# Kernel optimization log

Hardware: AMD Instinct MI355X
Metric: run time of the kernel (lower is better)

The kernel has to match this reference:

```python
import jax, jax.numpy as jnp
import numpy as np

N_NODES = 100_000
DEG = 16
N_EDGES = N_NODES * DEG
NODE_F = 128
EDGE_F = 16
HID = 64
B = 64
K = DEG


def setup_inputs() -> dict:
    key = jax.random.key(0)
    ks = jax.random.split(key, 12)
    # node i's outgoing edges are at ids i + k*N_NODES for k in [0, DEG)
    src = jnp.arange(N_EDGES, dtype=jnp.int32) % N_NODES
    dst = jax.random.randint(ks[0], (N_EDGES,), 0, N_NODES, dtype=jnp.int32)
    edge_index = jnp.stack([src, dst])
    current_nodes = jax.random.randint(ks[1], (B,), 0, N_NODES, dtype=jnp.int32)
    # reachable neighbors = destinations of the current node's real edges
    neighbor_nodes = dst[current_nodes[:, None] + jnp.arange(K, dtype=jnp.int32)[None, :] * N_NODES]
    x = jax.random.normal(ks[2], (N_NODES, NODE_F), jnp.float32)
    edge_attr = jax.random.normal(ks[3], (N_EDGES, EDGE_F), jnp.float32)
    return dict(
        x=x,
        edge_attr=edge_attr,
        conv1_W=jax.random.normal(ks[4], (NODE_F, HID), jnp.float32) * (NODE_F ** -0.5),
        conv1_b=jnp.zeros((HID,), jnp.float32),
        conv2_W=jax.random.normal(ks[5], (HID, HID), jnp.float32) * (HID ** -0.5),
        conv2_b=jnp.zeros((HID,), jnp.float32),
        mlp_W1=jax.random.normal(ks[6], (2 * HID + EDGE_F, 2 * HID), jnp.float32) * ((2 * HID + EDGE_F) ** -0.5),
        mlp_b1=jnp.zeros((2 * HID,), jnp.float32),
        mlp_W2=jax.random.normal(ks[7], (2 * HID, 1), jnp.float32) * ((2 * HID) ** -0.5),
        mlp_b2=jnp.zeros((1,), jnp.float32),
        edge_index=edge_index,
        current_nodes=current_nodes,
        neighbor_nodes=neighbor_nodes,
    )


def gcn_conv(x, edge_index, W, b):
    """PyG GCNConv: symmetric norm with self-loops, then linear + bias."""
    n = x.shape[0]
    loop = jnp.arange(n, dtype=edge_index.dtype)
    src = jnp.concatenate([edge_index[0], loop])  # messages flow src -> dst
    dst = jnp.concatenate([edge_index[1], loop])
    xw = x @ W                                    # [N, H]
    deg = jnp.zeros((n,), xw.dtype).at[dst].add(1.0)
    dinv = jnp.where(deg > 0, jax.lax.rsqrt(deg), 0.0)
    msg = (dinv[src] * dinv[dst])[:, None] * xw[src]      # [E+N, H]
    return jax.ops.segment_sum(msg, dst, num_segments=n) + b


def reference(x, edge_attr, conv1_W, conv1_b, conv2_W, conv2_b,
              mlp_W1, mlp_b1, mlp_W2, mlp_b2,
              edge_index, current_nodes, neighbor_nodes):
    n = x.shape[0]
    h = jax.nn.relu(gcn_conv(x, edge_index, conv1_W, conv1_b))
    h = jax.nn.relu(gcn_conv(h, edge_index, conv2_W, conv2_b))

    # First edge id matching each (current, neighbor) pair, replacing the
    # original O(E)-per-neighbor boolean-mask loop with a sorted-key lookup.
    keys = edge_index[0].astype(jnp.int64) * n + edge_index[1].astype(jnp.int64)
    order = jnp.argsort(keys, stable=True)        # stable -> leftmost == first edge id
    skeys = keys[order]
    query = current_nodes[:, None].astype(jnp.int64) * n + neighbor_nodes.astype(jnp.int64)
    pos = jnp.clip(jnp.searchsorted(skeys, query), 0, skeys.shape[0] - 1)
    valid = skeys[pos] == query                   # [B, K]
    eid = order[pos]
    ea = edge_attr[eid]                           # [B, K, F]

    b_, k_ = neighbor_nodes.shape
    h_cur = jnp.broadcast_to(h[current_nodes][:, None, :], (b_, k_, h.shape[1]))
    h_nbr = h[neighbor_nodes]
    m = jnp.concatenate([h_cur, h_nbr, ea], axis=-1)  # [B, K, 2H+F]
    q = (jax.nn.relu(m @ mlp_W1 + mlp_b1) @ mlp_W2 + mlp_b2)[..., 0]
    q = jnp.where(valid, q, 0.0)
    return q, valid
```

## Files before the change

kernel.cpp:

```cpp
#include <hip/hip_runtime.h>

#define N_NODES 100000
#define DEG 16
#define N_EDGES (N_NODES * DEG)
#define NODE_F 128
#define EDGE_F 16
#define HID 64
#define NQ 1024
#define NCHUNK (N_EDGES / 256)
#define XTILES ((N_NODES + 63) / 64)
#define BCAP 56
#define NODE_BLOCKS (N_NODES / 4)

__global__ void k_query(const int* __restrict__ dst, const int* __restrict__ cur,
                        const int* __restrict__ nbr, int* __restrict__ n1,
                        int* __restrict__ n2, int* __restrict__ eid_sel,
                        float* __restrict__ out_valid) {
  int i = blockIdx.x * blockDim.x + threadIdx.x;
  if (i >= NQ) return;
  int b = i >> 4;
  int c = cur[b];
  int nb = nbr[i];
  int sel = -1;
  #pragma unroll
  for (int j = 0; j < DEG; ++j) {
    int e = c + j * N_NODES;
    if (sel < 0 && dst[e] == nb) sel = e;
  }
  eid_sel[i] = sel;
  out_valid[i] = (sel >= 0) ? 1.0f : 0.0f;
  n2[c] = 1; n2[nb] = 1;
  n1[c] = 1; n1[nb] = 1;
}

__global__ void k_scan(const int* __restrict__ dst, const int* __restrict__ n2,
                       int* __restrict__ n1, int* __restrict__ deg) {
  int e = blockIdx.x * blockDim.x + threadIdx.x;
  if (e >= N_EDGES) return;
  int d = dst[e];
  atomicAdd(&deg[d], 1);
  if (n2[d]) n1[e % N_NODES] = 1;
}

__global__ void k_dinv(const int* __restrict__ deg, float* __restrict__ dinv) {
  int v = blockIdx.x * blockDim.x + threadIdx.x;
  if (v < N_NODES) dinv[v] = rsqrtf((float)(deg[v] + 1));
}

__global__ void k_bucket(const int* __restrict__ dst, const int* __restrict__ n1,
                         int* __restrict__ wcur, int* __restrict__ bucket) {
  int e = blockIdx.x * blockDim.x + threadIdx.x;
  if (e >= N_EDGES) return;
  int d = dst[e];
  if (!n1[d]) return;
  int pos = atomicAdd(&wcur[d], 1);
  if (pos < BCAP) bucket[(size_t)d * BCAP + pos] = e % N_NODES;
}

__global__ __launch_bounds__(256) void k_xw1(const float* __restrict__ x,
                                             const float* __restrict__ Wg,
                                             float* __restrict__ xw) {
  __shared__ float xs[64 * 129];
  const int t = threadIdx.x;
  const int lane = t & 63;
  const int w = __builtin_amdgcn_readfirstlane(t >> 6);
  const long base = (long)blockIdx.x * 64;

  const float4* __restrict__ xv = (const float4*)x;
  #pragma unroll
  for (int p = 0; p < 8; ++p) {
    int f4 = p * 256 + t;
    int r = f4 >> 5;
    int c4 = f4 & 31;
    long gr = base + r;
    float4 v = make_float4(0.f, 0.f, 0.f, 0.f);
    if (gr < N_NODES) v = xv[gr * 32 + c4];
    float* d = &xs[r * 129 + (c4 << 2)];
    d[0] = v.x; d[1] = v.y; d[2] = v.z; d[3] = v.w;
  }
  __syncthreads();

  float acc[16];
  #pragma unroll
  for (int j = 0; j < 16; ++j) acc[j] = 0.f;
  const float* __restrict__ wp = Wg + w * 16;
  #pragma unroll 4
  for (int k = 0; k < NODE_F; ++k) {
    float xk = xs[lane * 129 + k];
    float wv[16];
    #pragma unroll
    for (int j = 0; j < 16; ++j) wv[j] = wp[k * HID + j];
    #pragma unroll
    for (int j = 0; j < 16; ++j) acc[j] = fmaf(xk, wv[j], acc[j]);
  }
  long gr = base + lane;
  if (gr < N_NODES) {
    float* __restrict__ op = xw + gr * HID + w * 16;
    #pragma unroll
    for (int j = 0; j < 16; ++j) op[j] = acc[j];
  }
}

__global__ void k_xw2(const float* __restrict__ h1, const float* __restrict__ Wg,
                      const int* __restrict__ n1, float* __restrict__ xw2) {
  const int lane = threadIdx.x & 63;
  const int row = (blockIdx.x * blockDim.x + threadIdx.x) >> 6;
  if (row >= N_NODES) return;
  if (!n1[row]) return;
  const float* __restrict__ hr = h1 + (size_t)row * HID;
  float acc = 0.f;
  #pragma unroll
  for (int k = 0; k < HID; ++k) acc = fmaf(hr[k], Wg[k * HID + lane], acc);
  xw2[(size_t)row * HID + lane] = acc;
}

__global__ __launch_bounds__(256) void k_gather(
    const int* __restrict__ bucket, const int* __restrict__ wcur,
    const int* __restrict__ flag, const float* __restrict__ dinv,
    const float* __restrict__ xw, const float* __restrict__ bias,
    float* __restrict__ hout) {
  const int t = threadIdx.x;
  const int lane = t & 63;
  const int v = blockIdx.x * 4 + (t >> 6);
  if (v >= N_NODES) return;
  if (!flag[v]) return;
  int n = wcur[v];
  if (n > BCAP) n = BCAP;
  int   s_l = (lane < n) ? bucket[(size_t)v * BCAP + lane] : 0;
  float w_l = (lane < n) ? dinv[s_l] : 0.f;
  float acc = 0.f;
  int j = 0;
  for (; j + 3 < n; j += 4) {
    int s0 = __shfl(s_l, j);
    int s1 = __shfl(s_l, j + 1);
    int s2 = __shfl(s_l, j + 2);
    int s3 = __shfl(s_l, j + 3);
    float a0 = xw[(size_t)s0 * HID + lane];
    float a1 = xw[(size_t)s1 * HID + lane];
    float a2 = xw[(size_t)s2 * HID + lane];
    float a3 = xw[(size_t)s3 * HID + lane];
    acc = fmaf(__shfl(w_l, j), a0, acc);
    acc = fmaf(__shfl(w_l, j + 1), a1, acc);
    acc = fmaf(__shfl(w_l, j + 2), a2, acc);
    acc = fmaf(__shfl(w_l, j + 3), a3, acc);
  }
  for (; j < n; ++j)
    acc = fmaf(__shfl(w_l, j), xw[(size_t)__shfl(s_l, j) * HID + lane], acc);
  float dv = dinv[v];
  acc = fmaf(dv, xw[(size_t)v * HID + lane], acc);
  hout[(size_t)v * HID + lane] = fmaxf(fmaf(dv, acc, bias[lane]), 0.f);
}

__global__ void k_mlp(const float* __restrict__ h2, const float* __restrict__ ea,
                      const float* __restrict__ W1, const float* __restrict__ b1,
                      const float* __restrict__ W2, const float* __restrict__ b2,
                      const int* __restrict__ cur, const int* __restrict__ nbr,
                      const int* __restrict__ eid_sel, float* __restrict__ out) {
  __shared__ float m[2 * HID + EDGE_F];
  __shared__ float red[128];
  const int q = blockIdx.x;
  const int t = threadIdx.x;
  const int eid = eid_sel[q];
  if (eid < 0) {
    if (t == 0) out[q] = 0.0f;
    return;
  }
  const int b = q >> 4;
  const int c = cur[b];
  const int nb = nbr[q];
  if (t < HID)    m[t] = h2[(size_t)c * HID + t];
  else            m[t] = h2[(size_t)nb * HID + (t - HID)];
  if (t < EDGE_F) m[2 * HID + t] = ea[(size_t)eid * EDGE_F + t];
  __syncthreads();
  float h = b1[t];
  #pragma unroll
  for (int j = 0; j < 2 * HID + EDGE_F; ++j) h = fmaf(m[j], W1[j * 128 + t], h);
  h = fmaxf(h, 0.f) * W2[t];
  red[t] = h;
  __syncthreads();
  if (t < 64) {
    float v = red[t] + red[t + 64];
    #pragma unroll
    for (int o = 32; o > 0; o >>= 1) v += __shfl_down(v, o);
    if (t == 0) out[q] = v + b2[0];
  }
}

extern "C" void kernel_launch(void* const* d_in, const int* in_sizes, int n_in,
                              void* d_out, int out_size, void* d_ws, size_t ws_size,
                              hipStream_t stream) {
  const float* x    = (const float*)d_in[0];
  const float* ea   = (const float*)d_in[1];
  const float* c1W  = (const float*)d_in[2];
  const float* c1b  = (const float*)d_in[3];
  const float* c2W  = (const float*)d_in[4];
  const float* c2b  = (const float*)d_in[5];
  const float* mW1  = (const float*)d_in[6];
  const float* mb1  = (const float*)d_in[7];
  const float* mW2  = (const float*)d_in[8];
  const float* mb2  = (const float*)d_in[9];
  const int*   eidx = (const int*)d_in[10];
  const int*   cur  = (const int*)d_in[11];
  const int*   nbr  = (const int*)d_in[12];
  const int* edst = eidx + N_EDGES;
  float* out = (float*)d_out;

  char* p = (char*)d_ws;
  auto alloc = [&](size_t bytes) -> void* {
    void* r = (void*)p;
    p += (bytes + 255) & ~(size_t)255;
    return r;
  };
  int*   deg     = (int*)alloc((size_t)N_NODES * 4);
  float* dinv    = (float*)alloc((size_t)N_NODES * 4);
  int*   n1      = (int*)alloc((size_t)N_NODES * 4);
  int*   n2      = (int*)alloc((size_t)N_NODES * 4);
  int*   wcur    = (int*)alloc((size_t)N_NODES * 4);
  int*   eid_sel = (int*)alloc((size_t)NQ * 4);
  int*   bucket  = (int*)alloc((size_t)N_NODES * BCAP * 4);
  float* xw1     = (float*)alloc((size_t)N_NODES * HID * 4);
  float* h1      = (float*)alloc((size_t)N_NODES * HID * 4);
  float* xw2     = (float*)alloc((size_t)N_NODES * HID * 4);
  float* h2      = xw1;

  hipMemsetAsync(deg, 0, (size_t)N_NODES * 4, stream);
  hipMemsetAsync(n1, 0, (size_t)N_NODES * 4, stream);
  hipMemsetAsync(n2, 0, (size_t)N_NODES * 4, stream);
  hipMemsetAsync(wcur, 0, (size_t)N_NODES * 4, stream);

  k_query<<<(NQ + 255) / 256, 256, 0, stream>>>(edst, cur, nbr, n1, n2, eid_sel,
                                                out + NQ);
  k_scan<<<NCHUNK, 256, 0, stream>>>(edst, n2, n1, deg);
  k_dinv<<<(N_NODES + 255) / 256, 256, 0, stream>>>(deg, dinv);
  k_xw1<<<XTILES, 256, 0, stream>>>(x, c1W, xw1);
  k_bucket<<<NCHUNK, 256, 0, stream>>>(edst, n1, wcur, bucket);
  k_gather<<<NODE_BLOCKS, 256, 0, stream>>>(bucket, wcur, n1, dinv, xw1, c1b, h1);
  k_xw2<<<(N_NODES * HID + 255) / 256, 256, 0, stream>>>(h1, c2W, n1, xw2);
  k_gather<<<NODE_BLOCKS, 256, 0, stream>>>(bucket, wcur, n2, dinv, xw2, c2b, h2);
  k_mlp<<<NQ, 128, 0, stream>>>(h2, ea, mW1, mb1, mW2, mb2, cur, nbr, eid_sel, out);
}
```

Baseline: 380.4 us.

## Fuse graph preprocessing kernels, privatize degree histogram, replace flag memsets with sentinel

Four memsets and two separate launches are dropped. Node flags now use a magic sentinel value instead of being zeroed, and bucket counters are reset only for the nodes that get flagged. The degree histogram is split across 8 private copies, zeroed inside the query kernel, and computed in the same launch as the first-layer x@W GEMM so the two independent jobs overlap. The dinv computation shares a launch with bucketing. The aim is to cut launch and memset overhead and atomic contention, at the cost of relying on stale workspace never holding the sentinel and of leaving flags from earlier calls in place.

```diff
diff --git a/kernel.cpp b/kernel.cpp
--- a/kernel.cpp
+++ b/kernel.cpp
@@ -9,14 +9,25 @@
 #define NQ 1024
 #define NCHUNK (N_EDGES / 256)
 #define XTILES ((N_NODES + 63) / 64)
+#define NHIST 4096
 #define BCAP 56
-#define NODE_BLOCKS (N_NODES / 4)
-
-__global__ void k_query(const int* __restrict__ dst, const int* __restrict__ cur,
-                        const int* __restrict__ nbr, int* __restrict__ n1,
-                        int* __restrict__ n2, int* __restrict__ eid_sel,
-                        float* __restrict__ out_valid) {
-  int i = blockIdx.x * blockDim.x + threadIdx.x;
+#define NDINV ((N_NODES + 255) / 256)
+#define MAGIC 0x13579BDF
+
+__global__ void k_query_zero(const int* __restrict__ dst, const int* __restrict__ cur,
+                             const int* __restrict__ nbr, int* __restrict__ n1,
+                             int* __restrict__ n2, int* __restrict__ wcur,
+                             int* __restrict__ eid_sel, float* __restrict__ out_valid,
+                             int* __restrict__ degp) {
+  if (blockIdx.x >= 4) {
+    int4* d4 = (int4*)degp;
+    const int n4 = 8 * N_NODES / 4;
+    int i = (blockIdx.x - 4) * 256 + threadIdx.x;
+    const int stride = (gridDim.x - 4) * 256;
+    for (; i < n4; i += stride) d4[i] = make_int4(0, 0, 0, 0);
+    return;
+  }
+  int i = blockIdx.x * 256 + threadIdx.x;
   if (i >= NQ) return;
   int b = i >> 4;
   int c = cur[b];
@@ -29,42 +40,36 @@
   }
   eid_sel[i] = sel;
   out_valid[i] = (sel >= 0) ? 1.0f : 0.0f;
-  n2[c] = 1; n2[nb] = 1;
-  n1[c] = 1; n1[nb] = 1;
-}
-
-__global__ void k_scan(const int* __restrict__ dst, const int* __restrict__ n2,
-                       int* __restrict__ n1, int* __restrict__ deg) {
-  int e = blockIdx.x * blockDim.x + threadIdx.x;
-  if (e >= N_EDGES) return;
-  int d = dst[e];
-  atomicAdd(&deg[d], 1);
-  if (n2[d]) n1[e % N_NODES] = 1;
-}
-
-__global__ void k_dinv(const int* __restrict__ deg, float* __restrict__ dinv) {
-  int v = blockIdx.x * blockDim.x + threadIdx.x;
-  if (v < N_NODES) dinv[v] = rsqrtf((float)(deg[v] + 1));
-}
-
-__global__ void k_bucket(const int* __restrict__ dst, const int* __restrict__ n1,
-                         int* __restrict__ wcur, int* __restrict__ bucket) {
-  int e = blockIdx.x * blockDim.x + threadIdx.x;
-  if (e >= N_EDGES) return;
-  int d = dst[e];
-  if (!n1[d]) return;
-  int pos = atomicAdd(&wcur[d], 1);
-  if (pos < BCAP) bucket[(size_t)d * BCAP + pos] = e % N_NODES;
-}
-
-__global__ __launch_bounds__(256) void k_xw1(const float* __restrict__ x,
-                                             const float* __restrict__ Wg,
-                                             float* __restrict__ xw) {
+  n2[c] = MAGIC; n2[nb] = MAGIC;
+  n1[c] = MAGIC; n1[nb] = MAGIC;
+  wcur[c] = 0;   wcur[nb] = 0;
+}
+
+__global__ __launch_bounds__(256) void k_fusedA(
+    const float* __restrict__ x, const float* __restrict__ Wg,
+    float* __restrict__ xw, const int* __restrict__ dst,
+    const int* __restrict__ n2, int* __restrict__ n1, int* __restrict__ wcur,
+    int* __restrict__ degp) {
   __shared__ float xs[64 * 129];
   const int t = threadIdx.x;
+
+  if (blockIdx.x < NHIST) {
+    int* __restrict__ dp = degp + (size_t)(blockIdx.x & 7) * N_NODES;
+    for (int e = blockIdx.x * 256 + t; e < N_EDGES; e += NHIST * 256) {
+      int d = dst[e];
+      atomicAdd(&dp[d], 1);
+      if (n2[d] == MAGIC) {
+        int s = e % N_NODES;
+        n1[s] = MAGIC;
+        wcur[s] = 0;
+      }
+    }
+    return;
+  }
+
   const int lane = t & 63;
   const int w = __builtin_amdgcn_readfirstlane(t >> 6);
-  const long base = (long)blockIdx.x * 64;
+  const long base = (long)(blockIdx.x - NHIST) * 64;
 
   const float4* __restrict__ xv = (const float4*)x;
   #pragma unroll
@@ -101,12 +106,33 @@
   }
 }
 
+__global__ void k_bucket_dinv(const int* __restrict__ dst, const int* __restrict__ n1,
+                              int* __restrict__ wcur, int* __restrict__ bucket,
+                              const int* __restrict__ degp, float* __restrict__ dinv) {
+  if (blockIdx.x < NDINV) {
+    int v = blockIdx.x * 256 + threadIdx.x;
+    if (v < N_NODES) {
+      int s = 1;
+      #pragma unroll
+      for (int p = 0; p < 8; ++p) s += degp[(size_t)p * N_NODES + v];
+      dinv[v] = rsqrtf((float)s);
+    }
+    return;
+  }
+  int e = (blockIdx.x - NDINV) * 256 + threadIdx.x;
+  int d = dst[e];
+  if (n1[d] != MAGIC) return;
+  int pos = atomicAdd(&wcur[d], 1);
+  if (pos >= 0 && pos < BCAP)
+    bucket[(size_t)d * BCAP + pos] = e % N_NODES;
+}
+
 __global__ void k_xw2(const float* __restrict__ h1, const float* __restrict__ Wg,
                       const int* __restrict__ n1, float* __restrict__ xw2) {
   const int lane = threadIdx.x & 63;
   const int row = (blockIdx.x * blockDim.x + threadIdx.x) >> 6;
   if (row >= N_NODES) return;
-  if (!n1[row]) return;
+  if (n1[row] != MAGIC) return;
   const float* __restrict__ hr = h1 + (size_t)row * HID;
   float acc = 0.f;
   #pragma unroll
@@ -123,9 +149,10 @@
   const int lane = t & 63;
   const int v = blockIdx.x * 4 + (t >> 6);
   if (v >= N_NODES) return;
-  if (!flag[v]) return;
+  if (flag[v] != MAGIC) return;
   int n = wcur[v];
   if (n > BCAP) n = BCAP;
+  if (n < 0) n = 0;
   int   s_l = (lane < n) ? bucket[(size_t)v * BCAP + lane] : 0;
   float w_l = (lane < n) ? dinv[s_l] : 0.f;
   float acc = 0.f;
@@ -211,7 +238,7 @@
     p += (bytes + 255) & ~(size_t)255;
     return r;
   };
-  int*   deg     = (int*)alloc((size_t)N_NODES * 4);
+  int*   degp    = (int*)alloc((size_t)8 * N_NODES * 4);
   float* dinv    = (float*)alloc((size_t)N_NODES * 4);
   int*   n1      = (int*)alloc((size_t)N_NODES * 4);
   int*   n2      = (int*)alloc((size_t)N_NODES * 4);
@@ -223,19 +250,16 @@
   float* xw2     = (float*)alloc((size_t)N_NODES * HID * 4);
   float* h2      = xw1;
 
-  hipMemsetAsync(deg, 0, (size_t)N_NODES * 4, stream);
-  hipMemsetAsync(n1, 0, (size_t)N_NODES * 4, stream);
-  hipMemsetAsync(n2, 0, (size_t)N_NODES * 4, stream);
-  hipMemsetAsync(wcur, 0, (size_t)N_NODES * 4, stream);
-
-  k_query<<<(NQ + 255) / 256, 256, 0, stream>>>(edst, cur, nbr, n1, n2, eid_sel,
-                                                out + NQ);
-  k_scan<<<NCHUNK, 256, 0, stream>>>(edst, n2, n1, deg);
-  k_dinv<<<(N_NODES + 255) / 256, 256, 0, stream>>>(deg, dinv);
-  k_xw1<<<XTILES, 256, 0, stream>>>(x, c1W, xw1);
-  k_bucket<<<NCHUNK, 256, 0, stream>>>(edst, n1, wcur, bucket);
-  k_gather<<<NODE_BLOCKS, 256, 0, stream>>>(bucket, wcur, n1, dinv, xw1, c1b, h1);
+  k_query_zero<<<260, 256, 0, stream>>>(edst, cur, nbr, n1, n2, wcur, eid_sel,
+                                        out + NQ, degp);
+  k_fusedA<<<NHIST + XTILES, 256, 0, stream>>>(x, c1W, xw1, edst, n2, n1, wcur,
+                                               degp);
+  k_bucket_dinv<<<NDINV + NCHUNK, 256, 0, stream>>>(edst, n1, wcur, bucket, degp,
+                                                    dinv);
+  k_gather<<<(N_NODES + 3) / 4, 256, 0, stream>>>(bucket, wcur, n1, dinv, xw1,
+                                                  c1b, h1);
   k_xw2<<<(N_NODES * HID + 255) / 256, 256, 0, stream>>>(h1, c2W, n1, xw2);
-  k_gather<<<NODE_BLOCKS, 256, 0, stream>>>(bucket, wcur, n2, dinv, xw2, c2b, h2);
+  k_gather<<<(N_NODES + 3) / 4, 256, 0, stream>>>(bucket, wcur, n2, dinv, xw2,
+                                                  c2b, h2);
   k_mlp<<<NQ, 128, 0, stream>>>(h2, ea, mW1, mb1, mW2, mb2, cur, nbr, eid_sel, out);
 }
```

After: 361.9 us. 1.05x faster.
